# Optimization experiments

Measured on AMD Instinct MI355X. Metric: run time of the kernel, lower is better.

## Reference

```python
import jax, jax.numpy as jnp
import numpy as np

NUM_CLASSES = 10
BATCH = 2048
DIM = 128
TEMPERATURE = 0.07
BASE_TEMPERATURE = 0.07


def setup_inputs() -> dict:
    key = jax.random.key(0)
    k1, k2 = jax.random.split(key)
    preds = jax.random.normal(k1, (NUM_CLASSES, BATCH, DIM), dtype=jnp.float32)
    target = jax.random.randint(k2, (BATCH,), 0, NUM_CLASSES, dtype=jnp.int64)
    log_vars = jnp.zeros((NUM_CLASSES,), dtype=jnp.float32)
    return {"preds": preds, "target": target, "log_vars": log_vars}


def _per_class_loss(features, labels_bin):
    # features: [B, D], labels_bin: [B] in {0,1} (target == class i)
    B = features.shape[0]
    mask = (labels_bin[:, None] == labels_bin[None, :]).astype(features.dtype)  # [B,B]
    logits_mask = 1.0 - jnp.eye(B, dtype=features.dtype)                        # zero diagonal
    sim = jnp.matmul(features, features.T) / TEMPERATURE                        # [B,B]
    norms = jnp.linalg.norm(features, axis=1, keepdims=True)                    # [B,1]
    logits = sim / (norms * norms.T)                                            # cosine / temp
    mask = mask * logits_mask
    exp_logits = jnp.exp(logits) * logits_mask
    log_prob = logits - jnp.log(exp_logits.sum(axis=1, keepdims=True))
    mean_log_prob_pos = (mask * log_prob).sum(axis=1) / mask.sum(axis=1)
    loss = -(TEMPERATURE / BASE_TEMPERATURE) * mean_log_prob_pos
    return loss.mean()


def reference(preds, target, log_vars):
    # labels_bin[i] = (target == i), one row per class
    labels_bin = (target[None, :] == jnp.arange(NUM_CLASSES, dtype=target.dtype)[:, None])
    losses = jax.vmap(_per_class_loss)(preds, labels_bin)  # [num_classes]
    final_loss = jnp.sum(jnp.exp(-log_vars) * losses + log_vars)
    return final_loss
```

## Files before the change

kernel.cpp:

```cpp
#include <hip/hip_runtime.h>
#include <hip/hip_bf16.h>
#include <math.h>

#define NUM_CLASSES 10
#define BATCH 2048
#define DIM 128
#define INV_T 14.285714285714286f
#define NTILE 16
#define NPAIR 136

typedef __attribute__((ext_vector_type(8))) short bf16x8;
typedef __attribute__((ext_vector_type(4))) float f32x4;

__device__ __forceinline__ void load_lds16(const void* g, void* lds) {
    __builtin_amdgcn_global_load_lds(
        (const __attribute__((address_space(1))) unsigned int*)g,
        (__attribute__((address_space(3))) unsigned int*)lds,
        16, 0, 0);
}

__global__ __launch_bounds__(256) void normalize_kernel(
    const float* __restrict__ preds, __hip_bfloat16* __restrict__ g,
    float* __restrict__ zero_buf)
{
    int b = blockIdx.x;
    int t = threadIdx.x;
    if (t < 8) zero_buf[b * 8 + t] = 0.0f;

    int row  = b * 4 + (t >> 6);
    int lane = t & 63;
    const float2* src = (const float2*)(preds + (size_t)row * DIM);
    float2 v = src[lane];
    float ss = v.x * v.x + v.y * v.y;
#pragma unroll
    for (int m = 32; m; m >>= 1) ss += __shfl_xor(ss, m, 64);
    float rn = 1.0f / sqrtf(ss);
    __hip_bfloat162 o;
    o.x = __float2bfloat16(v.x * rn);
    o.y = __float2bfloat16(v.y * rn);
    *(__hip_bfloat162*)(g + (size_t)row * DIM + lane * 2) = o;
}

__global__ __launch_bounds__(256) void gram_kernel(
    const __hip_bfloat16* __restrict__ g, const int* __restrict__ target,
    float* __restrict__ denom, float* __restrict__ s2)
{
    int p = blockIdx.x;
    int by = 0, rem = NTILE;
    while (p >= rem) { p -= rem; --rem; ++by; }
    const int bx   = by + p;
    const int cls  = blockIdx.y;
    const int row0 = by * 128;
    const int col0 = bx * 128;
    const bool isDiag = (by == bx);
    const ushort* gc = (const ushort*)g + (size_t)cls * BATCH * DIM;

    __shared__ __align__(16) ushort smem[2 * 128 * 128];
    ushort* As = smem;
    ushort* Bs = smem + 128 * 128;

    const int t    = threadIdx.x;
    const int wid  = t >> 6;
    const int lane = t & 63;
    const int tx   = lane & 15;
    const int quad = lane >> 4;
    const int wm   = (wid >> 1) * 64;
    const int wn   = (wid & 1) * 64;

    const int lr = lane >> 4;
    const int lp = lane & 15;
#pragma unroll
    for (int s = 0; s < 8; ++s) {
        int rb = s * 16 + wid * 4;
        int r  = rb + lr;
        int c  = lp ^ (r & 15);
        load_lds16(gc + (size_t)(row0 + r) * DIM + c * 8, &As[rb * 128]);
        if (!isDiag)
            load_lds16(gc + (size_t)(col0 + r) * DIM + c * 8, &Bs[rb * 128]);
    }
    __syncthreads();

    const ushort* BsR = isDiag ? As : Bs;
    f32x4 acc[4][4] = {};
#pragma unroll
    for (int ks = 0; ks < 4; ++ks) {
        bf16x8 af[4], bg[4];
#pragma unroll
        for (int i = 0; i < 4; ++i) {
            int pa = ((ks * 4 + quad) ^ tx) * 8;
            af[i] = *(const bf16x8*)&As [(wm + i * 16 + tx) * 128 + pa];
            bg[i] = *(const bf16x8*)&BsR[(wn + i * 16 + tx) * 128 + pa];
        }
#pragma unroll
        for (int i = 0; i < 4; ++i)
#pragma unroll
            for (int j = 0; j < 4; ++j)
                acc[i][j] = __builtin_amdgcn_mfma_f32_16x16x32_bf16(
                    af[i], bg[j], acc[i][j], 0, 0, 0);
    }
    __syncthreads();

    unsigned laMask = 0;
#pragma unroll
    for (int i = 0; i < 4; ++i)
#pragma unroll
        for (int r = 0; r < 4; ++r)
            if (target[row0 + wm + i * 16 + quad * 4 + r] == cls)
                laMask |= 1u << (i * 4 + r);
    int lb[4];
#pragma unroll
    for (int j = 0; j < 4; ++j) lb[j] = (target[col0 + wn + j * 16 + tx] == cls);

    float2* rbuf = (float2*)smem;
    float2* cbuf = (float2*)(smem + 17408);
    float2 pcol[4] = {};

#pragma unroll
    for (int i = 0; i < 4; ++i) {
        float2 prow[4] = {};
#pragma unroll
        for (int j = 0; j < 4; ++j) {
            int cg = col0 + wn + j * 16 + tx;
            int lbj = lb[j];
#pragma unroll
            for (int r = 0; r < 4; ++r) {
                int rg = row0 + wm + i * 16 + quad * 4 + r;
                float logit = acc[i][j][r] * INV_T;
                float e = __expf(logit);
                bool dg = isDiag && (cg == rg);
                e = dg ? 0.0f : e;
                bool same = (((laMask >> (i * 4 + r)) & 1) == (unsigned)lbj) && !dg;
                float sl = same ? logit : 0.0f;
                prow[r].x += e; prow[r].y += sl;
                pcol[j].x += e; pcol[j].y += sl;
            }
        }
#pragma unroll
        for (int r = 0; r < 4; ++r)
            rbuf[wid * 1088 + (i * 16 + quad * 4 + r) * 17 + tx] = prow[r];
    }
#pragma unroll
    for (int j = 0; j < 4; ++j)
        cbuf[wid * 320 + (j * 16 + tx) * 5 + quad] = pcol[j];
    __syncthreads();

    if (t < 128) {
        int rl = t & 63, grp = t >> 6;
        float den = 0.0f, sp = 0.0f;
#pragma unroll
        for (int w = 0; w < 2; ++w) {
            int base = (2 * grp + w) * 1088 + rl * 17;
#pragma unroll
            for (int x = 0; x < 16; ++x) {
                float2 v = rbuf[base + x];
                den += v.x; sp += v.y;
            }
        }
        atomicAdd(&denom[cls * BATCH + row0 + t], den);
        atomicAdd(&s2   [cls * BATCH + row0 + t], sp);
    } else if (!isDiag) {
        int u = t - 128;
        int cl = u & 63, grp = u >> 6;
        float den = 0.0f, sp = 0.0f;
#pragma unroll
        for (int w = 0; w < 2; ++w) {
            int base = (grp + 2 * w) * 320 + cl * 5;
#pragma unroll
            for (int q = 0; q < 4; ++q) {
                float2 v = cbuf[base + q];
                den += v.x; sp += v.y;
            }
        }
        atomicAdd(&denom[cls * BATCH + col0 + u], den);
        atomicAdd(&s2   [cls * BATCH + col0 + u], sp);
    }
}

__global__ __launch_bounds__(1024) void final_kernel(
    const float* __restrict__ denom, const float* __restrict__ s2,
    const int* __restrict__ target, const float* __restrict__ log_vars,
    float* __restrict__ out)
{
    __shared__ int counts[NUM_CLASSES];
    __shared__ float wsum[16];
    int t = threadIdx.x;
    if (t < NUM_CLASSES) counts[t] = 0;
    __syncthreads();
    for (int i = t; i < BATCH; i += 1024) atomicAdd(&counts[target[i]], 1);
    __syncthreads();

    float partial = 0.0f;
    for (int idx = t; idx < NUM_CLASSES * BATCH; idx += 1024) {
        int i = idx >> 11;
        int a = idx & (BATCH - 1);
        int cnt = (target[a] == i) ? (counts[i] - 1) : (BATCH - counts[i] - 1);
        float mlpp = s2[idx] / (float)cnt - logf(denom[idx]);
        partial += __expf(-log_vars[i]) * mlpp;
    }
#pragma unroll
    for (int m = 32; m; m >>= 1) partial += __shfl_xor(partial, m, 64);
    if ((t & 63) == 0) wsum[t >> 6] = partial;
    __syncthreads();
    if (t == 0) {
        float tot = 0.0f;
        for (int w = 0; w < 16; ++w) tot += wsum[w];
        float lvsum = 0.0f;
        for (int i = 0; i < NUM_CLASSES; ++i) lvsum += log_vars[i];
        out[0] = -tot / (float)BATCH + lvsum;
    }
}

extern "C" void kernel_launch(void* const* d_in, const int* in_sizes, int n_in,
                              void* d_out, int out_size, void* d_ws, size_t ws_size,
                              hipStream_t stream)
{
    const float* preds    = (const float*)d_in[0];
    const int*   target   = (const int*)  d_in[1];
    const float* log_vars = (const float*)d_in[2];
    float* out = (float*)d_out;

    __hip_bfloat16* gbf = (__hip_bfloat16*)d_ws;
    float* denom = (float*)((char*)d_ws + (size_t)NUM_CLASSES * BATCH * DIM * 2);
    float* s2    = denom + (size_t)NUM_CLASSES * BATCH;

    normalize_kernel<<<NUM_CLASSES * BATCH / 4, 256, 0, stream>>>(preds, gbf, denom);
    gram_kernel<<<dim3(NPAIR, NUM_CLASSES), 256, 0, stream>>>(gbf, target, denom, s2);
    final_kernel<<<1, 1024, 0, stream>>>(denom, s2, target, log_vars, out);
}
```

Measured before the change: 91.88 us.

## Load MFMA operands directly from global and reduce partials via LDS atomics

The gram kernel no longer stages the 128x128 bf16 tiles in 64KB of shared memory. Each wave now reads its MFMA fragments straight from global memory, relying on L1/L2 reuse. The row and column partial-sum buffers are replaced with small shared arrays updated by LDS atomicAdd. This cuts LDS use and one barrier, which should raise occupancy, at the cost of redundant global loads across waves and contention on the LDS atomics.

```diff
diff --git a/kernel.cpp b/kernel.cpp
--- a/kernel.cpp
+++ b/kernel.cpp
@@ -11,13 +11,6 @@
 
 typedef __attribute__((ext_vector_type(8))) short bf16x8;
 typedef __attribute__((ext_vector_type(4))) float f32x4;
-
-__device__ __forceinline__ void load_lds16(const void* g, void* lds) {
-    __builtin_amdgcn_global_load_lds(
-        (const __attribute__((address_space(1))) unsigned int*)g,
-        (__attribute__((address_space(3))) unsigned int*)lds,
-        16, 0, 0);
-}
 
 __global__ __launch_bounds__(256) void normalize_kernel(
     const float* __restrict__ preds, __hip_bfloat16* __restrict__ g,
@@ -55,10 +48,6 @@
     const bool isDiag = (by == bx);
     const ushort* gc = (const ushort*)g + (size_t)cls * BATCH * DIM;
 
-    __shared__ __align__(16) ushort smem[2 * 128 * 128];
-    ushort* As = smem;
-    ushort* Bs = smem + 128 * 128;
-
     const int t    = threadIdx.x;
     const int wid  = t >> 6;
     const int lane = t & 63;
@@ -67,30 +56,19 @@
     const int wm   = (wid >> 1) * 64;
     const int wn   = (wid & 1) * 64;
 
-    const int lr = lane >> 4;
-    const int lp = lane & 15;
-#pragma unroll
-    for (int s = 0; s < 8; ++s) {
-        int rb = s * 16 + wid * 4;
-        int r  = rb + lr;
-        int c  = lp ^ (r & 15);
-        load_lds16(gc + (size_t)(row0 + r) * DIM + c * 8, &As[rb * 128]);
-        if (!isDiag)
-            load_lds16(gc + (size_t)(col0 + r) * DIM + c * 8, &Bs[rb * 128]);
-    }
-    __syncthreads();
+    const ushort* aBase = gc + (size_t)(row0 + wm + tx) * DIM + quad * 8;
+    const ushort* bBase = gc + (size_t)(col0 + wn + tx) * DIM + quad * 8;
 
-    const ushort* BsR = isDiag ? As : Bs;
     f32x4 acc[4][4] = {};
 #pragma unroll
     for (int ks = 0; ks < 4; ++ks) {
         bf16x8 af[4], bg[4];
 #pragma unroll
-        for (int i = 0; i < 4; ++i) {
-            int pa = ((ks * 4 + quad) ^ tx) * 8;
-            af[i] = *(const bf16x8*)&As [(wm + i * 16 + tx) * 128 + pa];
-            bg[i] = *(const bf16x8*)&BsR[(wn + i * 16 + tx) * 128 + pa];
-        }
+        for (int i = 0; i < 4; ++i)
+            af[i] = *(const bf16x8*)(aBase + i * 16 * DIM + ks * 32);
+#pragma unroll
+        for (int j = 0; j < 4; ++j)
+            bg[j] = *(const bf16x8*)(bBase + j * 16 * DIM + ks * 32);
 #pragma unroll
         for (int i = 0; i < 4; ++i)
 #pragma unroll
@@ -98,7 +76,10 @@
                 acc[i][j] = __builtin_amdgcn_mfma_f32_16x16x32_bf16(
                     af[i], bg[j], acc[i][j], 0, 0, 0);
     }
-    __syncthreads();
+
+    __shared__ float rowDen[128], rowSp[128], colDen[128], colSp[128];
+    if (t < 128) { rowDen[t] = 0.0f; rowSp[t] = 0.0f; }
+    else         { colDen[t - 128] = 0.0f; colSp[t - 128] = 0.0f; }
 
     unsigned laMask = 0;
 #pragma unroll
@@ -110,69 +91,50 @@
     int lb[4];
 #pragma unroll
     for (int j = 0; j < 4; ++j) lb[j] = (target[col0 + wn + j * 16 + tx] == cls);
+    __syncthreads();
 
-    float2* rbuf = (float2*)smem;
-    float2* cbuf = (float2*)(smem + 17408);
-    float2 pcol[4] = {};
-
+    float cden[4] = {}, csp[4] = {};
 #pragma unroll
     for (int i = 0; i < 4; ++i) {
-        float2 prow[4] = {};
 #pragma unroll
-        for (int j = 0; j < 4; ++j) {
-            int cg = col0 + wn + j * 16 + tx;
-            int lbj = lb[j];
+        for (int r = 0; r < 4; ++r) {
+            int rloc = wm + i * 16 + quad * 4 + r;
+            int rg = row0 + rloc;
+            unsigned la = (laMask >> (i * 4 + r)) & 1;
+            float den = 0.0f, sp = 0.0f;
 #pragma unroll
-            for (int r = 0; r < 4; ++r) {
-                int rg = row0 + wm + i * 16 + quad * 4 + r;
+            for (int j = 0; j < 4; ++j) {
+                int cg = col0 + wn + j * 16 + tx;
                 float logit = acc[i][j][r] * INV_T;
                 float e = __expf(logit);
                 bool dg = isDiag && (cg == rg);
                 e = dg ? 0.0f : e;
-                bool same = (((laMask >> (i * 4 + r)) & 1) == (unsigned)lbj) && !dg;
+                bool same = (la == (unsigned)lb[j]) && !dg;
                 float sl = same ? logit : 0.0f;
-                prow[r].x += e; prow[r].y += sl;
-                pcol[j].x += e; pcol[j].y += sl;
+                den += e; sp += sl;
+                cden[j] += e; csp[j] += sl;
             }
+            atomicAdd(&rowDen[rloc], den);
+            atomicAdd(&rowSp[rloc], sp);
         }
+    }
+    if (!isDiag) {
 #pragma unroll
-        for (int r = 0; r < 4; ++r)
-            rbuf[wid * 1088 + (i * 16 + quad * 4 + r) * 17 + tx] = prow[r];
+        for (int j = 0; j < 4; ++j) {
+            int cloc = wn + j * 16 + tx;
+            atomicAdd(&colDen[cloc], cden[j]);
+            atomicAdd(&colSp[cloc], csp[j]);
+        }
     }
-#pragma unroll
-    for (int j = 0; j < 4; ++j)
-        cbuf[wid * 320 + (j * 16 + tx) * 5 + quad] = pcol[j];
     __syncthreads();
 
     if (t < 128) {
-        int rl = t & 63, grp = t >> 6;
-        float den = 0.0f, sp = 0.0f;
-#pragma unroll
-        for (int w = 0; w < 2; ++w) {
-            int base = (2 * grp + w) * 1088 + rl * 17;
-#pragma unroll
-            for (int x = 0; x < 16; ++x) {
-                float2 v = rbuf[base + x];
-                den += v.x; sp += v.y;
-            }
-        }
-        atomicAdd(&denom[cls * BATCH + row0 + t], den);
-        atomicAdd(&s2   [cls * BATCH + row0 + t], sp);
+        atomicAdd(&denom[cls * BATCH + row0 + t], rowDen[t]);
+        atomicAdd(&s2   [cls * BATCH + row0 + t], rowSp[t]);
     } else if (!isDiag) {
         int u = t - 128;
-        int cl = u & 63, grp = u >> 6;
-        float den = 0.0f, sp = 0.0f;
-#pragma unroll
-        for (int w = 0; w < 2; ++w) {
-            int base = (grp + 2 * w) * 320 + cl * 5;
-#pragma unroll
-            for (int q = 0; q < 4; ++q) {
-                float2 v = cbuf[base + q];
-                den += v.x; sp += v.y;
-            }
-        }
-        atomicAdd(&denom[cls * BATCH + col0 + u], den);
-        atomicAdd(&s2   [cls * BATCH + col0 + u], sp);
+        atomicAdd(&denom[cls * BATCH + col0 + u], colDen[u]);
+        atomicAdd(&s2   [cls * BATCH + col0 + u], colSp[u]);
     }
 }
 
```

New measurement: 181.4 us. 1.97x slower.

## Compute positive-logit sums via per-label feature sums instead of inside Gram tiles

Applied to the files above, without the earlier changes.

The sum of same-label logits for each row is rewritten algebraically as a dot product between that row and the sum of normalized features sharing its label, minus the self term. A new gsum kernel builds the per-label feature sums and class counts. This lets the Gram kernel drop the target loads, the label masks and the second accumulator and atomic. The final reduction is also spread across many blocks instead of one. The cost is an extra launch and a serial 256-row loop in a 10-block kernel, plus a bf16 dot-product approximation of the positive-logit sum.

```diff
diff --git a/kernel.cpp b/kernel.cpp
--- a/kernel.cpp
+++ b/kernel.cpp
@@ -41,9 +41,52 @@
     *(__hip_bfloat162*)(g + (size_t)row * DIM + lane * 2) = o;
 }
 
+__global__ __launch_bounds__(1024) void gsum_kernel(
+    const __hip_bfloat16* __restrict__ g, const int* __restrict__ target,
+    const float* __restrict__ log_vars, float* __restrict__ Gsum,
+    int* __restrict__ counts, float* __restrict__ out)
+{
+    const int cls = blockIdx.x;
+    const int t = threadIdx.x;
+    const int d = t & 127, sl = t >> 7;
+    const __hip_bfloat16* gc = g + (size_t)cls * BATCH * DIM;
+
+    float a0 = 0.0f, a1 = 0.0f;
+    int c1 = 0;
+    for (int r8 = 0; r8 < 256; ++r8) {
+        int row = sl * 256 + r8;
+        int lbl = target[row];
+        float v = __bfloat162float(gc[(size_t)row * DIM + d]);
+        if (lbl == cls) { a1 += v; ++c1; } else { a0 += v; }
+    }
+    __shared__ float red[2][8][128];
+    __shared__ int cpart[8];
+    red[0][sl][d] = a0;
+    red[1][sl][d] = a1;
+    if (d == 0) cpart[sl] = c1;
+    __syncthreads();
+    if (t < 256) {
+        int h = t >> 7, dd = t & 127;
+        float s = 0.0f;
+#pragma unroll
+        for (int k = 0; k < 8; ++k) s += red[h][k][dd];
+        Gsum[cls * 256 + h * 128 + dd] = s;
+    }
+    if (t == 0) {
+        int c = 0;
+#pragma unroll
+        for (int k = 0; k < 8; ++k) c += cpart[k];
+        counts[cls] = c;
+        if (cls == 0) {
+            float lv = 0.0f;
+            for (int i = 0; i < NUM_CLASSES; ++i) lv += log_vars[i];
+            out[0] = lv;
+        }
+    }
+}
+
 __global__ __launch_bounds__(256) void gram_kernel(
-    const __hip_bfloat16* __restrict__ g, const int* __restrict__ target,
-    float* __restrict__ denom, float* __restrict__ s2)
+    const __hip_bfloat16* __restrict__ g, float* __restrict__ denom)
 {
     int p = blockIdx.x;
     int by = 0, rem = NTILE;
@@ -100,114 +143,103 @@
     }
     __syncthreads();
 
-    unsigned laMask = 0;
-#pragma unroll
-    for (int i = 0; i < 4; ++i)
-#pragma unroll
-        for (int r = 0; r < 4; ++r)
-            if (target[row0 + wm + i * 16 + quad * 4 + r] == cls)
-                laMask |= 1u << (i * 4 + r);
-    int lb[4];
-#pragma unroll
-    for (int j = 0; j < 4; ++j) lb[j] = (target[col0 + wn + j * 16 + tx] == cls);
-
-    float2* rbuf = (float2*)smem;
-    float2* cbuf = (float2*)(smem + 17408);
-    float2 pcol[4] = {};
+    float* rbuf = (float*)smem;
+    float* cbuf = (float*)smem + 4 * 1088;
+    float cden[4] = {};
 
 #pragma unroll
     for (int i = 0; i < 4; ++i) {
-        float2 prow[4] = {};
-#pragma unroll
-        for (int j = 0; j < 4; ++j) {
-            int cg = col0 + wn + j * 16 + tx;
-            int lbj = lb[j];
-#pragma unroll
-            for (int r = 0; r < 4; ++r) {
+#pragma unroll
+        for (int r = 0; r < 4; ++r) {
+            float den = 0.0f;
+            if (isDiag) {
                 int rg = row0 + wm + i * 16 + quad * 4 + r;
-                float logit = acc[i][j][r] * INV_T;
-                float e = __expf(logit);
-                bool dg = isDiag && (cg == rg);
-                e = dg ? 0.0f : e;
-                bool same = (((laMask >> (i * 4 + r)) & 1) == (unsigned)lbj) && !dg;
-                float sl = same ? logit : 0.0f;
-                prow[r].x += e; prow[r].y += sl;
-                pcol[j].x += e; pcol[j].y += sl;
+#pragma unroll
+                for (int j = 0; j < 4; ++j) {
+                    int cg = col0 + wn + j * 16 + tx;
+                    float e = __expf(acc[i][j][r] * INV_T);
+                    e = (cg == rg) ? 0.0f : e;
+                    den += e; cden[j] += e;
+                }
+            } else {
+#pragma unroll
+                for (int j = 0; j < 4; ++j) {
+                    float e = __expf(acc[i][j][r] * INV_T);
+                    den += e; cden[j] += e;
+                }
             }
-        }
-#pragma unroll
-        for (int r = 0; r < 4; ++r)
-            rbuf[wid * 1088 + (i * 16 + quad * 4 + r) * 17 + tx] = prow[r];
+            rbuf[wid * 1088 + (i * 16 + quad * 4 + r) * 17 + tx] = den;
+        }
     }
 #pragma unroll
     for (int j = 0; j < 4; ++j)
-        cbuf[wid * 320 + (j * 16 + tx) * 5 + quad] = pcol[j];
+        cbuf[wid * 320 + (j * 16 + tx) * 5 + quad] = cden[j];
     __syncthreads();
 
     if (t < 128) {
         int rl = t & 63, grp = t >> 6;
-        float den = 0.0f, sp = 0.0f;
+        float den = 0.0f;
 #pragma unroll
         for (int w = 0; w < 2; ++w) {
             int base = (2 * grp + w) * 1088 + rl * 17;
 #pragma unroll
-            for (int x = 0; x < 16; ++x) {
-                float2 v = rbuf[base + x];
-                den += v.x; sp += v.y;
-            }
+            for (int x = 0; x < 16; ++x) den += rbuf[base + x];
         }
         atomicAdd(&denom[cls * BATCH + row0 + t], den);
-        atomicAdd(&s2   [cls * BATCH + row0 + t], sp);
     } else if (!isDiag) {
-        int u = t - 128;
-        int cl = u & 63, grp = u >> 6;
-        float den = 0.0f, sp = 0.0f;
+        int u = t - 128, cl = u & 63, grp = u >> 6;
+        float den = 0.0f;
 #pragma unroll
         for (int w = 0; w < 2; ++w) {
             int base = (grp + 2 * w) * 320 + cl * 5;
 #pragma unroll
-            for (int q = 0; q < 4; ++q) {
-                float2 v = cbuf[base + q];
-                den += v.x; sp += v.y;
-            }
+            for (int q = 0; q < 4; ++q) den += cbuf[base + q];
         }
         atomicAdd(&denom[cls * BATCH + col0 + u], den);
-        atomicAdd(&s2   [cls * BATCH + col0 + u], sp);
-    }
-}
-
-__global__ __launch_bounds__(1024) void final_kernel(
-    const float* __restrict__ denom, const float* __restrict__ s2,
+    }
+}
+
+__global__ __launch_bounds__(256) void final_kernel(
+    const __hip_bfloat16* __restrict__ g, const float* __restrict__ denom,
     const int* __restrict__ target, const float* __restrict__ log_vars,
+    const float* __restrict__ Gsum, const int* __restrict__ counts,
     float* __restrict__ out)
 {
-    __shared__ int counts[NUM_CLASSES];
-    __shared__ float wsum[16];
-    int t = threadIdx.x;
-    if (t < NUM_CLASSES) counts[t] = 0;
-    __syncthreads();
-    for (int i = t; i < BATCH; i += 1024) atomicAdd(&counts[target[i]], 1);
-    __syncthreads();
-
-    float partial = 0.0f;
-    for (int idx = t; idx < NUM_CLASSES * BATCH; idx += 1024) {
-        int i = idx >> 11;
-        int a = idx & (BATCH - 1);
-        int cnt = (target[a] == i) ? (counts[i] - 1) : (BATCH - counts[i] - 1);
-        float mlpp = s2[idx] / (float)cnt - logf(denom[idx]);
-        partial += __expf(-log_vars[i]) * mlpp;
-    }
-#pragma unroll
-    for (int m = 32; m; m >>= 1) partial += __shfl_xor(partial, m, 64);
-    if ((t & 63) == 0) wsum[t >> 6] = partial;
-    __syncthreads();
-    if (t == 0) {
-        float tot = 0.0f;
-        for (int w = 0; w < 16; ++w) tot += wsum[w];
-        float lvsum = 0.0f;
-        for (int i = 0; i < NUM_CLASSES; ++i) lvsum += log_vars[i];
-        out[0] = -tot / (float)BATCH + lvsum;
-    }
+    __shared__ float gs[256];
+    __shared__ float wred[4];
+    const int t   = threadIdx.x;
+    const int idx = blockIdx.x * 256 + t;
+    const int cls = idx >> 11;
+    const int a   = idx & (BATCH - 1);
+
+    gs[t] = Gsum[cls * 256 + t];
+    __syncthreads();
+
+    const int la = (target[a] == cls) ? 1 : 0;
+    const bf16x8* rp = (const bf16x8*)((const ushort*)g + ((size_t)cls * BATCH + a) * DIM);
+    const float* gv = &gs[la * 128];
+    float dot = 0.0f;
+#pragma unroll
+    for (int k = 0; k < 16; ++k) {
+        bf16x8 v = rp[k];
+#pragma unroll
+        for (int e = 0; e < 8; ++e) {
+            union { unsigned u; float f; } cv;
+            cv.u = ((unsigned)(unsigned short)v[e]) << 16;
+            dot += cv.f * gv[k * 8 + e];
+        }
+    }
+    int c1  = counts[cls];
+    int cnt = la ? (c1 - 1) : (BATCH - c1 - 1);
+    float s2v  = (dot - 1.0f) * INV_T;
+    float mlpp = s2v / (float)cnt - logf(denom[idx]);
+    float part = __expf(-log_vars[cls]) * mlpp;
+#pragma unroll
+    for (int m = 32; m; m >>= 1) part += __shfl_xor(part, m, 64);
+    if ((t & 63) == 0) wred[t >> 6] = part;
+    __syncthreads();
+    if (t == 0)
+        atomicAdd(out, -(wred[0] + wred[1] + wred[2] + wred[3]) / (float)BATCH);
 }
 
 extern "C" void kernel_launch(void* const* d_in, const int* in_sizes, int n_in,
@@ -221,9 +253,12 @@
 
     __hip_bfloat16* gbf = (__hip_bfloat16*)d_ws;
     float* denom = (float*)((char*)d_ws + (size_t)NUM_CLASSES * BATCH * DIM * 2);
-    float* s2    = denom + (size_t)NUM_CLASSES * BATCH;
+    float* Gsum  = denom + 40960;
+    int*   counts = (int*)(Gsum + NUM_CLASSES * 256);
 
     normalize_kernel<<<NUM_CLASSES * BATCH / 4, 256, 0, stream>>>(preds, gbf, denom);
-    gram_kernel<<<dim3(NPAIR, NUM_CLASSES), 256, 0, stream>>>(gbf, target, denom, s2);
-    final_kernel<<<1, 1024, 0, stream>>>(denom, s2, target, log_vars, out);
-}
+    gsum_kernel<<<NUM_CLASSES, 1024, 0, stream>>>(gbf, target, log_vars, Gsum, counts, out);
+    gram_kernel<<<dim3(NPAIR, NUM_CLASSES), 256, 0, stream>>>(gbf, denom);
+    final_kernel<<<NUM_CLASSES * BATCH / 256, 256, 0, stream>>>(
+        gbf, denom, target, log_vars, Gsum, counts, out);
+}
```

Measured after the change: 102.7 us. 11.8% more time.
